# Kernel tuning notes

Hardware: AMD Instinct MI355X
Metric: run time of the kernel (lower is better)

## Reference

```python
import jax, jax.numpy as jnp
import numpy as np

SPATIAL_SHAPES = [(128, 128), (64, 64), (32, 32), (16, 16)]  # (H_l, W_l) per level
NUM_HEADS = 8
NUM_LEVELS = 4
NUM_POINTS = 4
EMBED_DIM = 256
HEAD_DIM = EMBED_DIM // NUM_HEADS
LEN_V = sum(h * w for h, w in SPATIAL_SHAPES)  # 21760
BS, LQ = 8, 900


def setup_inputs() -> dict:
    key = jax.random.key(0)
    ks = jax.random.split(key, 12)
    s = 0.05
    return {
        'query': jax.random.normal(ks[0], (BS, LQ, EMBED_DIM), jnp.float32),
        'reference_points': jax.random.uniform(ks[1], (BS, LQ, NUM_LEVELS, 2), jnp.float32),
        'value': jax.random.normal(ks[2], (BS, LEN_V, EMBED_DIM), jnp.float32),
        'w_value': jax.random.normal(ks[3], (EMBED_DIM, EMBED_DIM), jnp.float32) * s,
        'b_value': jnp.zeros((EMBED_DIM,), jnp.float32),
        'w_off': jax.random.normal(ks[4], (EMBED_DIM, NUM_HEADS * NUM_LEVELS * NUM_POINTS * 2), jnp.float32) * s,
        'b_off': jax.random.normal(ks[5], (NUM_HEADS * NUM_LEVELS * NUM_POINTS * 2,), jnp.float32),
        'w_attn': jax.random.normal(ks[6], (EMBED_DIM, NUM_HEADS * NUM_LEVELS * NUM_POINTS), jnp.float32) * s,
        'b_attn': jnp.zeros((NUM_HEADS * NUM_LEVELS * NUM_POINTS,), jnp.float32),
        'w_out': jax.random.normal(ks[7], (EMBED_DIM, EMBED_DIM), jnp.float32) * s,
        'b_out': jnp.zeros((EMBED_DIM,), jnp.float32),
    }


def _bilinear_sample(val, locx, locy, H, W):
    # val: [bs, nh, H*W, hd]; locx/locy: [bs, nh, N] normalized in [0,1]
    # grid_sample semantics: align_corners=False, zero padding.
    px = locx * W - 0.5
    py = locy * H - 0.5
    x0 = jnp.floor(px)
    y0 = jnp.floor(py)
    dx = px - x0
    dy = py - y0
    x0i = x0.astype(jnp.int32)
    y0i = y0.astype(jnp.int32)
    out = jnp.zeros(val.shape[:2] + (locx.shape[-1], val.shape[-1]), val.dtype)
    corners = [
        (x0i, y0i, (1 - dx) * (1 - dy)),
        (x0i + 1, y0i, dx * (1 - dy)),
        (x0i, y0i + 1, (1 - dx) * dy),
        (x0i + 1, y0i + 1, dx * dy),
    ]
    for xi, yi, w in corners:
        valid = ((xi >= 0) & (xi < W) & (yi >= 0) & (yi < H)).astype(val.dtype)
        idx = jnp.clip(yi, 0, H - 1) * W + jnp.clip(xi, 0, W - 1)
        g = jnp.take_along_axis(val, idx[..., None], axis=2)  # [bs,nh,N,hd]
        out = out + g * (w * valid)[..., None]
    return out


def reference(query, reference_points, value, w_value, b_value, w_off, b_off,
              w_attn, b_attn, w_out, b_out):
    bs, Lq, C = query.shape
    # value projection -> [bs, Lv, nh, hd]
    v = (value @ w_value + b_value).reshape(bs, -1, NUM_HEADS, HEAD_DIM)
    # sampling offsets [bs,Lq,nh,L,P,2], attention weights softmax over L*P
    off = (query @ w_off + b_off).reshape(bs, Lq, NUM_HEADS, NUM_LEVELS, NUM_POINTS, 2)
    aw = (query @ w_attn + b_attn).reshape(bs, Lq, NUM_HEADS, NUM_LEVELS * NUM_POINTS)
    aw = jax.nn.softmax(aw, axis=-1).reshape(bs, Lq, NUM_HEADS, NUM_LEVELS, NUM_POINTS)
    # normalizer is (W_l, H_l) per level (flip of spatial shapes)
    norm = jnp.asarray([[w, h] for h, w in SPATIAL_SHAPES], query.dtype)  # [L,2]
    loc = reference_points[:, :, None, :, None, :] + off / norm[None, None, None, :, None, :]
    # per-level bilinear sampling and weighted reduction
    out = jnp.zeros((bs, Lq, NUM_HEADS, HEAD_DIM), query.dtype)
    start = 0
    for l, (H, W) in enumerate(SPATIAL_SHAPES):
        vl = v[:, start:start + H * W]                       # [bs,HW,nh,hd]
        vl = vl.transpose(0, 2, 1, 3)                        # [bs,nh,HW,hd]
        ll = loc[:, :, :, l].transpose(0, 2, 1, 3, 4)        # [bs,nh,Lq,P,2]
        ll = ll.reshape(bs, NUM_HEADS, Lq * NUM_POINTS, 2)
        s = _bilinear_sample(vl, ll[..., 0], ll[..., 1], H, W)
        s = s.reshape(bs, NUM_HEADS, Lq, NUM_POINTS, HEAD_DIM)
        out = out + jnp.einsum('bhqpd,bqhp->bqhd', s, aw[:, :, :, l])
        start += H * W
    out = out.reshape(bs, Lq, C)
    return out @ w_out + b_out
```

## Files before the change

### kernel.cpp

```cpp
#include <hip/hip_runtime.h>

#define BS 8
#define LQ 900
#define NH 8
#define NL 4
#define NP 4
#define HD 32
#define ED 256
#define LEN_V 21760

#define QB 32
#define QCHUNKS 29

typedef __attribute__((ext_vector_type(8))) short bf16x8;
typedef __attribute__((ext_vector_type(4))) float f32x4;
typedef __attribute__((ext_vector_type(4))) float fv4;

static __device__ __forceinline__ unsigned short f2bf(float f) {
  union { float f; unsigned u; } x; x.f = f;
  unsigned r = x.u + 0x7fffu + ((x.u >> 16) & 1u);
  return (unsigned short)(r >> 16);
}
static __device__ __forceinline__ float bf_lo(unsigned u) {
  union { unsigned u; float f; } x; x.u = u << 16;
  return x.f;
}
static __device__ __forceinline__ float bf_hi(unsigned u) {
  union { unsigned u; float f; } x; x.u = u & 0xffff0000u;
  return x.f;
}
static __device__ __forceinline__ unsigned pack2(float a, float b) {
  return (unsigned)f2bf(a) | ((unsigned)f2bf(b) << 16);
}

__global__ __launch_bounds__(256) void bprep_kernel(
    const float* __restrict__ w, unsigned short* __restrict__ Bsw) {
  const int id = blockIdx.x * 256 + threadIdx.x;
  const int n = id & 255;
  const int kseg = (id >> 8) & 3;
  const int kc = id >> 10;
  const float* src = &w[(kc * 32 + kseg * 8) * 256 + n];
  float f[8];
#pragma unroll
  for (int j = 0; j < 8; j++) f[j] = src[j * 256];
  uint4 pk;
  pk.x = pack2(f[0], f[1]);
  pk.y = pack2(f[2], f[3]);
  pk.z = pack2(f[4], f[5]);
  pk.w = pack2(f[6], f[7]);
  *(uint4*)&Bsw[((kc * 4 + kseg) * 256 + n) * 8] = pk;
}

__global__ __launch_bounds__(256, 4) void vproj_kernel(
    const float* __restrict__ value, const unsigned short* __restrict__ Bsw,
    const float* __restrict__ bias, unsigned short* __restrict__ vout) {
  const int t = threadIdx.x;
  const int row0 = blockIdx.x * 64;
  const int wv = t >> 6;
  const int lane = t & 63;
  const int quad = lane >> 4;
  const int nn = lane & 15;

  __shared__ unsigned short a_lds[4 * 64 * 8];

  f32x4 acc[4][4];
#pragma unroll
  for (int i = 0; i < 4; i++)
#pragma unroll
    for (int j = 0; j < 4; j++) acc[i][j] = (f32x4)(0.f);

  const int arow = t >> 2;
  const int akseg = t & 3;
  const unsigned short* bptr = &Bsw[(quad * 256 + wv * 64 + nn) * 8];

  for (int kc = 0; kc < 8; kc++) {
    __syncthreads();
    {
      const float* pa = &value[(row0 + arow) * 256 + kc * 32 + akseg * 8];
      fv4 v0 = __builtin_nontemporal_load((const fv4*)pa);
      fv4 v1 = __builtin_nontemporal_load((const fv4*)(pa + 4));
      uint4 pk;
      pk.x = pack2(v0.x, v0.y);
      pk.y = pack2(v0.z, v0.w);
      pk.z = pack2(v1.x, v1.y);
      pk.w = pack2(v1.z, v1.w);
      *(uint4*)&a_lds[(akseg * 64 + arow) * 8] = pk;
    }
    __syncthreads();

    bf16x8 af[4], bfr[4];
#pragma unroll
    for (int ct = 0; ct < 4; ct++)
      bfr[ct] = *(const bf16x8*)(bptr + (kc * 1024 + ct * 16) * 8);
#pragma unroll
    for (int rt = 0; rt < 4; rt++)
      af[rt] = *(const bf16x8*)&a_lds[(quad * 64 + rt * 16 + nn) * 8];
#pragma unroll
    for (int rt = 0; rt < 4; rt++)
#pragma unroll
      for (int ct = 0; ct < 4; ct++)
        acc[rt][ct] = __builtin_amdgcn_mfma_f32_16x16x32_bf16(
            af[rt], bfr[ct], acc[rt][ct], 0, 0, 0);
  }

  const int bb = row0 / LEN_V;
  const int s0 = row0 - bb * LEN_V;
#pragma unroll
  for (int ct = 0; ct < 4; ct++) {
    const int col = wv * 64 + ct * 16 + nn;
    const float bv = bias[col];
    const int h = col >> 5;
    const int d = col & 31;
    unsigned short* vb = &vout[((bb * NH + h) * LEN_V + s0) * HD + d];
#pragma unroll
    for (int rt = 0; rt < 4; rt++) {
      f32x4 f = acc[rt][ct];
#pragma unroll
      for (int reg = 0; reg < 4; reg++) {
        const int s = rt * 16 + quad * 4 + reg;
        vb[s * HD] = f2bf(f[reg] + bv);
      }
    }
  }
}

__global__ __launch_bounds__(384, 2) void offattn_kernel(
    const float* __restrict__ query,
    const float* __restrict__ w_off, const float* __restrict__ b_off,
    const float* __restrict__ w_attn, const float* __restrict__ b_attn,
    float* __restrict__ OFF, float* __restrict__ LOG) {
  const int t = threadIdx.x;
  const int row0 = blockIdx.x * 32;
  const int rg = t / 96;
  const int c4 = t % 96;
  const int col = c4 * 4;
  const bool isOff = col < 256;
  const float* wbase = isOff ? (w_off + col) : (w_attn + (col - 256));
  const int wstride = isOff ? 256 : 128;
  const float* bb = isOff ? (b_off + col) : (b_attn + (col - 256));
  __shared__ float a_lds[32][8];

  float4 acc[8];
#pragma unroll
  for (int r = 0; r < 8; r++) acc[r] = make_float4(0.f, 0.f, 0.f, 0.f);

  for (int k0 = 0; k0 < 256; k0 += 8) {
    __syncthreads();
    if (t < 256) a_lds[t >> 3][t & 7] = query[(row0 + (t >> 3)) * 256 + k0 + (t & 7)];
    __syncthreads();
    float4 wr[8];
#pragma unroll
    for (int k = 0; k < 8; k++)
      wr[k] = *(const float4*)&wbase[(k0 + k) * wstride];
#pragma unroll
    for (int r = 0; r < 8; r++) {
      const float* ar = &a_lds[rg * 8 + r][0];
      float4 a0 = *(const float4*)&ar[0];
      float4 a1 = *(const float4*)&ar[4];
      float4 s = acc[r];
      s.x += a0.x*wr[0].x + a0.y*wr[1].x + a0.z*wr[2].x + a0.w*wr[3].x
           + a1.x*wr[4].x + a1.y*wr[5].x + a1.z*wr[6].x + a1.w*wr[7].x;
      s.y += a0.x*wr[0].y + a0.y*wr[1].y + a0.z*wr[2].y + a0.w*wr[3].y
           + a1.x*wr[4].y + a1.y*wr[5].y + a1.z*wr[6].y + a1.w*wr[7].y;
      s.z += a0.x*wr[0].z + a0.y*wr[1].z + a0.z*wr[2].z + a0.w*wr[3].z
           + a1.x*wr[4].z + a1.y*wr[5].z + a1.z*wr[6].z + a1.w*wr[7].z;
      s.w += a0.x*wr[0].w + a0.y*wr[1].w + a0.z*wr[2].w + a0.w*wr[3].w
           + a1.x*wr[4].w + a1.y*wr[5].w + a1.z*wr[6].w + a1.w*wr[7].w;
      acc[r] = s;
    }
  }

  const float4 bv = *(const float4*)bb;
#pragma unroll
  for (int r = 0; r < 8; r++) {
    const int grow = row0 + rg * 8 + r;
    float4 o = make_float4(acc[r].x + bv.x, acc[r].y + bv.y,
                           acc[r].z + bv.z, acc[r].w + bv.w);
    if (isOff) *(float4*)&OFF[grow * 256 + col] = o;
    else       *(float4*)&LOG[grow * 128 + (col - 256)] = o;
  }
}

__global__ __launch_bounds__(256, 6) void sample_kernel(
    const float* __restrict__ refp, const unsigned short* __restrict__ vp,
    const float* __restrict__ OFF, const float* __restrict__ LOG,
    float* __restrict__ RES) {
  const int t = threadIdx.x;
  const int work = (blockIdx.x & 7) * (8 * QCHUNKS) + (blockIdx.x >> 3);
  const int pair = work / QCHUNKS;
  const int qc   = work - pair * QCHUNKS;
  const int b = pair >> 3;
  const int h = pair & 7;
  const int q0 = qc * QB;

  __shared__ float off_lds[QB][32];
  __shared__ float aw_lds[QB][16];
  __shared__ float ref_lds[QB][4][2];
  __shared__ int   soff[QB * 16][4];
  __shared__ float swt[QB * 16][4];

#pragma unroll
  for (int rep = 0; rep < 4; rep++) {
    const int tt = t + rep * 256;
    const int q = tt >> 5, j = tt & 31;
    off_lds[q][j] = (q0 + q < LQ) ? OFF[(b * LQ + q0 + q) * 256 + h * 32 + j] : 0.f;
  }
#pragma unroll
  for (int rep = 0; rep < 2; rep++) {
    const int tt = t + rep * 256;
    const int q = tt >> 4, j = tt & 15;
    aw_lds[q][j] = (q0 + q < LQ) ? LOG[(b * LQ + q0 + q) * 128 + h * 16 + j] : 0.f;
  }
  {
    const int q = t >> 3, l = (t >> 1) & 3, xy = t & 1;
    ref_lds[q][l][xy] = (q0 + q < LQ)
        ? refp[((b * LQ + q0 + q) * NL + l) * 2 + xy] : 0.5f;
  }
  __syncthreads();

  if (t < QB) {
    float* a = &aw_lds[t][0];
    float m = a[0];
#pragma unroll
    for (int i = 1; i < 16; i++) m = fmaxf(m, a[i]);
    float e[16];
    float ssum = 0.f;
#pragma unroll
    for (int i = 0; i < 16; i++) { e[i] = __expf(a[i] - m); ssum += e[i]; }
    const float inv = 1.f / ssum;
#pragma unroll
    for (int i = 0; i < 16; i++) a[i] = e[i] * inv;
  }
  __syncthreads();

#pragma unroll
  for (int ss = 0; ss < 2; ss++) {
    const int sid = t + ss * 256;
    const int p = sid & 3, l = (sid >> 2) & 3, q = sid >> 4;
    const int W = 128 >> l;
    const int base = (l == 0) ? 0 : ((l == 1) ? 16384 : ((l == 2) ? 20480 : 21504));
    const float Wf = (float)W;
    const float refx = ref_lds[q][l][0];
    const float refy = ref_lds[q][l][1];
    const float offx = off_lds[q][l * 8 + p * 2 + 0];
    const float offy = off_lds[q][l * 8 + p * 2 + 1];
    const float aw = aw_lds[q][l * 4 + p];
    const float px = refx * Wf + offx - 0.5f;
    const float py = refy * Wf + offy - 0.5f;
    const float x0f = floorf(px), y0f = floorf(py);
    const float dx = px - x0f, dy = py - y0f;
    const int x0 = (int)x0f, y0 = (int)y0f;
    const int x1 = x0 + 1, y1 = y0 + 1;
    const float mx0 = (x0 >= 0 && x0 < W) ? 1.f : 0.f;
    const float mx1 = (x1 >= 0 && x1 < W) ? 1.f : 0.f;
    const float my0 = (y0 >= 0 && y0 < W) ? 1.f : 0.f;
    const float my1 = (y1 >= 0 && y1 < W) ? 1.f : 0.f;
    const int x0c = min(max(x0, 0), W - 1);
    const int x1c = min(max(x1, 0), W - 1);
    const int y0c = min(max(y0, 0), W - 1);
    const int y1c = min(max(y1, 0), W - 1);
    soff[sid][0] = (base + y0c * W + x0c) * 8;
    soff[sid][1] = (base + y0c * W + x1c) * 8;
    soff[sid][2] = (base + y1c * W + x0c) * 8;
    soff[sid][3] = (base + y1c * W + x1c) * 8;
    swt[sid][0] = (1.f - dx) * (1.f - dy) * mx0 * my0 * aw;
    swt[sid][1] = dx * (1.f - dy) * mx1 * my0 * aw;
    swt[sid][2] = (1.f - dx) * dy * mx0 * my1 * aw;
    swt[sid][3] = dx * dy * mx1 * my1 * aw;
  }
  __syncthreads();

  const int q = t >> 3;
  const int d4 = t & 7;
  const uint2* vpu2 = (const uint2*)vp + (size_t)(b * NH + h) * (LEN_V * HD / 4);
  float r0 = 0.f, r1 = 0.f, r2 = 0.f, r3 = 0.f;
  const int sbase = q << 4;
#pragma unroll 4
  for (int lp = 0; lp < 16; lp++) {
    const int sid = sbase + lp;
    const int4 o = *(const int4*)&soff[sid][0];
    const float4 w = *(const float4*)&swt[sid][0];
    const uint2 u00 = vpu2[o.x + d4];
    const uint2 u10 = vpu2[o.y + d4];
    const uint2 u01 = vpu2[o.z + d4];
    const uint2 u11 = vpu2[o.w + d4];
    r0 += w.x * bf_lo(u00.x) + w.y * bf_lo(u10.x) + w.z * bf_lo(u01.x) + w.w * bf_lo(u11.x);
    r1 += w.x * bf_hi(u00.x) + w.y * bf_hi(u10.x) + w.z * bf_hi(u01.x) + w.w * bf_hi(u11.x);
    r2 += w.x * bf_lo(u00.y) + w.y * bf_lo(u10.y) + w.z * bf_lo(u01.y) + w.w * bf_lo(u11.y);
    r3 += w.x * bf_hi(u00.y) + w.y * bf_hi(u10.y) + w.z * bf_hi(u01.y) + w.w * bf_hi(u11.y);
  }
  if (q0 + q < LQ) {
    float4 rr = make_float4(r0, r1, r2, r3);
    *(float4*)&RES[(b * LQ + q0 + q) * 256 + h * 32 + d4 * 4] = rr;
  }
}

__global__ __launch_bounds__(256, 2) void outproj_kernel(
    const float* __restrict__ RES, const float* __restrict__ w,
    const float* __restrict__ bias, float* __restrict__ out) {
  const int t = threadIdx.x;
  const int row0 = blockIdx.x * 32;
  const int rg = t >> 6;
  const int c0 = (t & 63) << 2;
  __shared__ float a_lds[32][8];

  float4 acc[8];
#pragma unroll
  for (int r = 0; r < 8; r++) acc[r] = make_float4(0.f, 0.f, 0.f, 0.f);

  const int lr = t >> 3;
  const int lk = t & 7;
  for (int k0 = 0; k0 < 256; k0 += 8) {
    __syncthreads();
    a_lds[lr][lk] = RES[(row0 + lr) * 256 + k0 + lk];
    __syncthreads();
    float4 wr[8];
#pragma unroll
    for (int k = 0; k < 8; k++)
      wr[k] = *(const float4*)&w[(k0 + k) * 256 + c0];
#pragma unroll
    for (int r = 0; r < 8; r++) {
      const float* ar = &a_lds[rg * 8 + r][0];
      float4 a0 = *(const float4*)&ar[0];
      float4 a1 = *(const float4*)&ar[4];
      float4 s = acc[r];
      s.x += a0.x*wr[0].x + a0.y*wr[1].x + a0.z*wr[2].x + a0.w*wr[3].x
           + a1.x*wr[4].x + a1.y*wr[5].x + a1.z*wr[6].x + a1.w*wr[7].x;
      s.y += a0.x*wr[0].y + a0.y*wr[1].y + a0.z*wr[2].y + a0.w*wr[3].y
           + a1.x*wr[4].y + a1.y*wr[5].y + a1.z*wr[6].y + a1.w*wr[7].y;
      s.z += a0.x*wr[0].z + a0.y*wr[1].z + a0.z*wr[2].z + a0.w*wr[3].z
           + a1.x*wr[4].z + a1.y*wr[5].z + a1.z*wr[6].z + a1.w*wr[7].z;
      s.w += a0.x*wr[0].w + a0.y*wr[1].w + a0.z*wr[2].w + a0.w*wr[3].w
           + a1.x*wr[4].w + a1.y*wr[5].w + a1.z*wr[6].w + a1.w*wr[7].w;
      acc[r] = s;
    }
  }

  const float4 bv = *(const float4*)&bias[c0];
#pragma unroll
  for (int r = 0; r < 8; r++) {
    const int grow = row0 + rg * 8 + r;
    float4 o = make_float4(acc[r].x + bv.x, acc[r].y + bv.y,
                           acc[r].z + bv.z, acc[r].w + bv.w);
    *(float4*)&out[grow * 256 + c0] = o;
  }
}

extern "C" void kernel_launch(void* const* d_in, const int* in_sizes, int n_in,
                              void* d_out, int out_size, void* d_ws, size_t ws_size,
                              hipStream_t stream) {
  (void)in_sizes; (void)n_in; (void)out_size; (void)ws_size;
  const float* query   = (const float*)d_in[0];
  const float* refp    = (const float*)d_in[1];
  const float* value   = (const float*)d_in[2];
  const float* w_value = (const float*)d_in[3];
  const float* b_value = (const float*)d_in[4];
  const float* w_off   = (const float*)d_in[5];
  const float* b_off   = (const float*)d_in[6];
  const float* w_attn  = (const float*)d_in[7];
  const float* b_attn  = (const float*)d_in[8];
  const float* w_out   = (const float*)d_in[9];
  const float* b_out   = (const float*)d_in[10];
  float* out = (float*)d_out;

  char* ws = (char*)d_ws;
  unsigned short* vp = (unsigned short*)ws;
  float* OFF = (float*)(ws + 89128960);
  float* LOG = (float*)(ws + 89128960 + 7372800);
  float* RES = (float*)(ws + 89128960 + 7372800 + 3686400);
  unsigned short* Bsw = (unsigned short*)(ws + 89128960 + 7372800 + 3686400 + 7372800);

  bprep_kernel<<<32, 256, 0, stream>>>(w_value, Bsw);
  vproj_kernel<<<(BS * LEN_V) / 64, 256, 0, stream>>>(value, Bsw, b_value, vp);
  offattn_kernel<<<(BS * LQ) / 32, 384, 0, stream>>>(query, w_off, b_off,
                                                     w_attn, b_attn, OFF, LOG);
  sample_kernel<<<64 * QCHUNKS, 256, 0, stream>>>(refp, vp, OFF, LOG, RES);
  outproj_kernel<<<(BS * LQ) / 32, 256, 0, stream>>>(RES, w_out, b_out, out);
}
```

Before: 417.5 us.

## Double-buffer LDS and prefetch next K-chunk in value projection GEMM

The value projection kernel now uses two LDS buffers and issues the global loads for the next K-chunk of A and the B fragments before running the MFMAs on the current chunk. This replaces two barriers per iteration with one and hides global load latency behind matrix compute. The extra registers for prefetched data led to lowering the occupancy hint in launch bounds from 4 to 3 blocks per CU, which may reduce latency hiding across waves.

```diff
diff --git a/kernel.cpp b/kernel.cpp
--- a/kernel.cpp
+++ b/kernel.cpp
@@ -51,7 +51,7 @@
   *(uint4*)&Bsw[((kc * 4 + kseg) * 256 + n) * 8] = pk;
 }
 
-__global__ __launch_bounds__(256, 4) void vproj_kernel(
+__global__ __launch_bounds__(256, 3) void vproj_kernel(
     const float* __restrict__ value, const unsigned short* __restrict__ Bsw,
     const float* __restrict__ bias, unsigned short* __restrict__ vout) {
   const int t = threadIdx.x;
@@ -61,7 +61,7 @@
   const int quad = lane >> 4;
   const int nn = lane & 15;
 
-  __shared__ unsigned short a_lds[4 * 64 * 8];
+  __shared__ unsigned short a_lds[2][4 * 64 * 8];
 
   f32x4 acc[4][4];
 #pragma unroll
@@ -71,36 +71,69 @@
 
   const int arow = t >> 2;
   const int akseg = t & 3;
+  const float* pa = &value[(row0 + arow) * 256 + akseg * 8];
   const unsigned short* bptr = &Bsw[(quad * 256 + wv * 64 + nn) * 8];
-
-  for (int kc = 0; kc < 8; kc++) {
-    __syncthreads();
+  unsigned short* awp0 = &a_lds[0][(akseg * 64 + arow) * 8];
+  const unsigned short* arp0 = &a_lds[0][(quad * 64 + nn) * 8];
+
+  bf16x8 bcur[4];
+#pragma unroll
+  for (int ct = 0; ct < 4; ct++)
+    bcur[ct] = *(const bf16x8*)(bptr + ct * 128);
+  {
+    fv4 v0 = __builtin_nontemporal_load((const fv4*)pa);
+    fv4 v1 = __builtin_nontemporal_load((const fv4*)(pa + 4));
+    uint4 pk;
+    pk.x = pack2(v0.x, v0.y);
+    pk.y = pack2(v0.z, v0.w);
+    pk.z = pack2(v1.x, v1.y);
+    pk.w = pack2(v1.z, v1.w);
+    *(uint4*)awp0 = pk;
+  }
+  __syncthreads();
+
+#pragma unroll 1
+  for (int kc = 0; kc < 7; kc++) {
+    const int cur = kc & 1;
+    fv4 n0 = __builtin_nontemporal_load((const fv4*)(pa + (kc + 1) * 32));
+    fv4 n1 = __builtin_nontemporal_load((const fv4*)(pa + (kc + 1) * 32 + 4));
+    bf16x8 bnext[4];
+#pragma unroll
+    for (int ct = 0; ct < 4; ct++)
+      bnext[ct] = *(const bf16x8*)(bptr + (kc + 1) * 8192 + ct * 128);
+    bf16x8 af[4];
+#pragma unroll
+    for (int rt = 0; rt < 4; rt++)
+      af[rt] = *(const bf16x8*)(arp0 + cur * 2048 + rt * 128);
+#pragma unroll
+    for (int rt = 0; rt < 4; rt++)
+#pragma unroll
+      for (int ct = 0; ct < 4; ct++)
+        acc[rt][ct] = __builtin_amdgcn_mfma_f32_16x16x32_bf16(
+            af[rt], bcur[ct], acc[rt][ct], 0, 0, 0);
     {
-      const float* pa = &value[(row0 + arow) * 256 + kc * 32 + akseg * 8];
-      fv4 v0 = __builtin_nontemporal_load((const fv4*)pa);
-      fv4 v1 = __builtin_nontemporal_load((const fv4*)(pa + 4));
       uint4 pk;
-      pk.x = pack2(v0.x, v0.y);
-      pk.y = pack2(v0.z, v0.w);
-      pk.z = pack2(v1.x, v1.y);
-      pk.w = pack2(v1.z, v1.w);
-      *(uint4*)&a_lds[(akseg * 64 + arow) * 8] = pk;
+      pk.x = pack2(n0.x, n0.y);
+      pk.y = pack2(n0.z, n0.w);
+      pk.z = pack2(n1.x, n1.y);
+      pk.w = pack2(n1.z, n1.w);
+      *(uint4*)(awp0 + (cur ^ 1) * 2048) = pk;
     }
     __syncthreads();
-
-    bf16x8 af[4], bfr[4];
-#pragma unroll
-    for (int ct = 0; ct < 4; ct++)
-      bfr[ct] = *(const bf16x8*)(bptr + (kc * 1024 + ct * 16) * 8);
+#pragma unroll
+    for (int ct = 0; ct < 4; ct++) bcur[ct] = bnext[ct];
+  }
+  {
+    bf16x8 af[4];
 #pragma unroll
     for (int rt = 0; rt < 4; rt++)
-      af[rt] = *(const bf16x8*)&a_lds[(quad * 64 + rt * 16 + nn) * 8];
+      af[rt] = *(const bf16x8*)(arp0 + 2048 + rt * 128);
 #pragma unroll
     for (int rt = 0; rt < 4; rt++)
 #pragma unroll
       for (int ct = 0; ct < 4; ct++)
         acc[rt][ct] = __builtin_amdgcn_mfma_f32_16x16x32_bf16(
-            af[rt], bfr[ct], acc[rt][ct], 0, 0, 0);
+            af[rt], bcur[ct], acc[rt][ct], 0, 0, 0);
   }
 
   const int bb = row0 / LEN_V;
```

New measurement: 425.6 us. About the same (+1.9%).

## Fuse offset/attention projection into sampling kernel per (batch, head, query chunk)

Applied to the files above, without the earlier changes.

Removes the separate offattn kernel and its OFF/LOG global buffers. Each sampling block now loads its 32 query rows into shared memory and computes only its head's 48 offset/logit columns directly into LDS, reusing the shared buffer for the sampling tables. This saves a kernel launch and the global round trip of the intermediates. In exchange the query rows are loaded once per head (8x redundant query reads), shared memory per block grows, and launch bounds drop from 6 to 4 blocks per CU.

```diff
diff --git a/kernel.cpp b/kernel.cpp
--- a/kernel.cpp
+++ b/kernel.cpp
@@ -124,66 +124,11 @@
   }
 }
 
-__global__ __launch_bounds__(384, 2) void offattn_kernel(
-    const float* __restrict__ query,
+__global__ __launch_bounds__(256, 4) void samp_kernel(
+    const float* __restrict__ query, const float* __restrict__ refp,
+    const unsigned short* __restrict__ vp,
     const float* __restrict__ w_off, const float* __restrict__ b_off,
     const float* __restrict__ w_attn, const float* __restrict__ b_attn,
-    float* __restrict__ OFF, float* __restrict__ LOG) {
-  const int t = threadIdx.x;
-  const int row0 = blockIdx.x * 32;
-  const int rg = t / 96;
-  const int c4 = t % 96;
-  const int col = c4 * 4;
-  const bool isOff = col < 256;
-  const float* wbase = isOff ? (w_off + col) : (w_attn + (col - 256));
-  const int wstride = isOff ? 256 : 128;
-  const float* bb = isOff ? (b_off + col) : (b_attn + (col - 256));
-  __shared__ float a_lds[32][8];
-
-  float4 acc[8];
-#pragma unroll
-  for (int r = 0; r < 8; r++) acc[r] = make_float4(0.f, 0.f, 0.f, 0.f);
-
-  for (int k0 = 0; k0 < 256; k0 += 8) {
-    __syncthreads();
-    if (t < 256) a_lds[t >> 3][t & 7] = query[(row0 + (t >> 3)) * 256 + k0 + (t & 7)];
-    __syncthreads();
-    float4 wr[8];
-#pragma unroll
-    for (int k = 0; k < 8; k++)
-      wr[k] = *(const float4*)&wbase[(k0 + k) * wstride];
-#pragma unroll
-    for (int r = 0; r < 8; r++) {
-      const float* ar = &a_lds[rg * 8 + r][0];
-      float4 a0 = *(const float4*)&ar[0];
-      float4 a1 = *(const float4*)&ar[4];
-      float4 s = acc[r];
-      s.x += a0.x*wr[0].x + a0.y*wr[1].x + a0.z*wr[2].x + a0.w*wr[3].x
-           + a1.x*wr[4].x + a1.y*wr[5].x + a1.z*wr[6].x + a1.w*wr[7].x;
-      s.y += a0.x*wr[0].y + a0.y*wr[1].y + a0.z*wr[2].y + a0.w*wr[3].y
-           + a1.x*wr[4].y + a1.y*wr[5].y + a1.z*wr[6].y + a1.w*wr[7].y;
-      s.z += a0.x*wr[0].z + a0.y*wr[1].z + a0.z*wr[2].z + a0.w*wr[3].z
-           + a1.x*wr[4].z + a1.y*wr[5].z + a1.z*wr[6].z + a1.w*wr[7].z;
-      s.w += a0.x*wr[0].w + a0.y*wr[1].w + a0.z*wr[2].w + a0.w*wr[3].w
-           + a1.x*wr[4].w + a1.y*wr[5].w + a1.z*wr[6].w + a1.w*wr[7].w;
-      acc[r] = s;
-    }
-  }
-
-  const float4 bv = *(const float4*)bb;
-#pragma unroll
-  for (int r = 0; r < 8; r++) {
-    const int grow = row0 + rg * 8 + r;
-    float4 o = make_float4(acc[r].x + bv.x, acc[r].y + bv.y,
-                           acc[r].z + bv.z, acc[r].w + bv.w);
-    if (isOff) *(float4*)&OFF[grow * 256 + col] = o;
-    else       *(float4*)&LOG[grow * 128 + (col - 256)] = o;
-  }
-}
-
-__global__ __launch_bounds__(256, 6) void sample_kernel(
-    const float* __restrict__ refp, const unsigned short* __restrict__ vp,
-    const float* __restrict__ OFF, const float* __restrict__ LOG,
     float* __restrict__ RES) {
   const int t = threadIdx.x;
   const int work = (blockIdx.x & 7) * (8 * QCHUNKS) + (blockIdx.x >> 3);
@@ -193,28 +138,78 @@
   const int h = pair & 7;
   const int q0 = qc * QB;
 
-  __shared__ float off_lds[QB][32];
-  __shared__ float aw_lds[QB][16];
-  __shared__ float ref_lds[QB][4][2];
-  __shared__ int   soff[QB * 16][4];
-  __shared__ float swt[QB * 16][4];
-
-#pragma unroll
-  for (int rep = 0; rep < 4; rep++) {
-    const int tt = t + rep * 256;
-    const int q = tt >> 5, j = tt & 31;
-    off_lds[q][j] = (q0 + q < LQ) ? OFF[(b * LQ + q0 + q) * 256 + h * 32 + j] : 0.f;
-  }
-#pragma unroll
-  for (int rep = 0; rep < 2; rep++) {
-    const int tt = t + rep * 256;
-    const int q = tt >> 4, j = tt & 15;
-    aw_lds[q][j] = (q0 + q < LQ) ? LOG[(b * LQ + q0 + q) * 128 + h * 16 + j] : 0.f;
+  __shared__ __align__(16) unsigned char smem[39936];
+  float* q_ldsf = (float*)smem;
+  int   (*soff)[4] = (int(*)[4])smem;
+  float (*swt)[4]  = (float(*)[4])(smem + 8192);
+  float (*off_lds)[32] = (float(*)[32])(smem + 32768);
+  float (*aw_lds)[16]  = (float(*)[16])(smem + 32768 + 4096);
+  float (*ref_lds)[4][2] = (float(*)[4][2])(smem + 32768 + 6144);
+
+#pragma unroll
+  for (int k = 0; k < 8; k++) {
+    const int f = t + k * 256;
+    const int row = f >> 6;
+    const int c4i = (f & 63) << 2;
+    float4 v = (q0 + row < LQ)
+        ? *(const float4*)&query[(b * LQ + q0 + row) * 256 + c4i]
+        : make_float4(0.f, 0.f, 0.f, 0.f);
+    *(float4*)&q_ldsf[row * 256 + c4i] = v;
   }
   {
     const int q = t >> 3, l = (t >> 1) & 3, xy = t & 1;
     ref_lds[q][l][xy] = (q0 + q < LQ)
         ? refp[((b * LQ + q0 + q) * NL + l) * 2 + xy] : 0.5f;
+  }
+  __syncthreads();
+
+  if (t < 192) {
+    const int rg = t / 12;
+    const int c4 = t % 12;
+    const int col = c4 * 4;
+    const bool isOff = col < 32;
+    const float* wbase = isOff ? (w_off + h * 32 + col)
+                               : (w_attn + h * 16 + (col - 32));
+    const int wstride = isOff ? 256 : 128;
+    const float* bb = isOff ? (b_off + h * 32 + col)
+                            : (b_attn + h * 16 + (col - 32));
+
+    float4 acc[2];
+    acc[0] = make_float4(0.f, 0.f, 0.f, 0.f);
+    acc[1] = make_float4(0.f, 0.f, 0.f, 0.f);
+
+    for (int k0 = 0; k0 < 256; k0 += 8) {
+      float4 wr[8];
+#pragma unroll
+      for (int k = 0; k < 8; k++)
+        wr[k] = *(const float4*)&wbase[(k0 + k) * wstride];
+#pragma unroll
+      for (int r = 0; r < 2; r++) {
+        const float* ar = &q_ldsf[(rg * 2 + r) * 256 + k0];
+        float4 a0 = *(const float4*)&ar[0];
+        float4 a1 = *(const float4*)&ar[4];
+        float4 s = acc[r];
+        s.x += a0.x*wr[0].x + a0.y*wr[1].x + a0.z*wr[2].x + a0.w*wr[3].x
+             + a1.x*wr[4].x + a1.y*wr[5].x + a1.z*wr[6].x + a1.w*wr[7].x;
+        s.y += a0.x*wr[0].y + a0.y*wr[1].y + a0.z*wr[2].y + a0.w*wr[3].y
+             + a1.x*wr[4].y + a1.y*wr[5].y + a1.z*wr[6].y + a1.w*wr[7].y;
+        s.z += a0.x*wr[0].z + a0.y*wr[1].z + a0.z*wr[2].z + a0.w*wr[3].z
+             + a1.x*wr[4].z + a1.y*wr[5].z + a1.z*wr[6].z + a1.w*wr[7].z;
+        s.w += a0.x*wr[0].w + a0.y*wr[1].w + a0.z*wr[2].w + a0.w*wr[3].w
+             + a1.x*wr[4].w + a1.y*wr[5].w + a1.z*wr[6].w + a1.w*wr[7].w;
+        acc[r] = s;
+      }
+    }
+
+    const float4 bv = *(const float4*)bb;
+#pragma unroll
+    for (int r = 0; r < 2; r++) {
+      const int q = rg * 2 + r;
+      float4 o = make_float4(acc[r].x + bv.x, acc[r].y + bv.y,
+                             acc[r].z + bv.z, acc[r].w + bv.w);
+      if (isOff) *(float4*)&off_lds[q][col] = o;
+      else       *(float4*)&aw_lds[q][col - 32] = o;
+    }
   }
   __syncthreads();
 
@@ -364,16 +359,14 @@
   float* out = (float*)d_out;
 
   char* ws = (char*)d_ws;
-  unsigned short* vp = (unsigned short*)ws;
-  float* OFF = (float*)(ws + 89128960);
-  float* LOG = (float*)(ws + 89128960 + 7372800);
-  float* RES = (float*)(ws + 89128960 + 7372800 + 3686400);
-  unsigned short* Bsw = (unsigned short*)(ws + 89128960 + 7372800 + 3686400 + 7372800);
+  unsigned short* vp  = (unsigned short*)ws;
+  float* RES          = (float*)(ws + 89128960);
+  unsigned short* Bsw = (unsigned short*)(ws + 89128960 + 7372800);
 
   bprep_kernel<<<32, 256, 0, stream>>>(w_value, Bsw);
   vproj_kernel<<<(BS * LEN_V) / 64, 256, 0, stream>>>(value, Bsw, b_value, vp);
-  offattn_kernel<<<(BS * LQ) / 32, 384, 0, stream>>>(query, w_off, b_off,
-                                                     w_attn, b_attn, OFF, LOG);
-  sample_kernel<<<64 * QCHUNKS, 256, 0, stream>>>(refp, vp, OFF, LOG, RES);
+  samp_kernel<<<64 * QCHUNKS, 256, 0, stream>>>(query, refp, vp,
+                                                w_off, b_off, w_attn, b_attn,
+                                                RES);
   outproj_kernel<<<(BS * LQ) / 32, 256, 0, stream>>>(RES, w_out, b_out, out);
 }
```

Result: no change. 412.0 us (-1.3%).
